# Performance work log

Hardware: AMD Instinct MI355X
Metric: run time of the kernel (lower is better)

## Reference

```python
import jax, jax.numpy as jnp
import numpy as np

D_MODEL = 1024
N_HEADS = 16
D_K = D_MODEL // N_HEADS
SEQ = 2048
BATCH = 2
THETA = 10000.0


def apply_rope(x, positions, theta):
    # x: [..., h, s, d_k], positions: [s]
    d_k = x.shape[-1]
    inv_freq = 1.0 / (theta ** (jnp.arange(0, d_k, 2, dtype=jnp.float32) / d_k))  # [d_k/2]
    ang = positions.astype(jnp.float32)[:, None] * inv_freq[None, :]  # [s, d_k/2]
    cos, sin = jnp.cos(ang), jnp.sin(ang)
    xe, xo = x[..., 0::2], x[..., 1::2]
    re = xe * cos - xo * sin
    ro = xe * sin + xo * cos
    return jnp.stack([re, ro], axis=-1).reshape(x.shape)


def setup_inputs() -> dict:
    key = jax.random.key(0)
    ks = jax.random.split(key, 7)
    f = lambda k, s: jax.random.normal(k, s, dtype=jnp.float32)
    return {
        "Q": f(ks[0], (BATCH, SEQ, D_MODEL)),
        "K": f(ks[1], (BATCH, SEQ, D_MODEL)),
        "V": f(ks[2], (BATCH, SEQ, D_MODEL)),
        "w_q": f(ks[3], (D_MODEL, D_MODEL)) * 0.02,
        "w_k": f(ks[4], (D_MODEL, D_MODEL)) * 0.02,
        "w_v": f(ks[5], (D_MODEL, D_MODEL)) * 0.02,
        "w_o": f(ks[6], (D_MODEL, D_MODEL)) * 0.02,
        "mask": jnp.tril(jnp.ones((SEQ, SEQ), dtype=bool)),
        "token_positions": jnp.arange(SEQ, dtype=jnp.int32),
    }


def reference(Q, K, V, w_q, w_k, w_v, w_o, mask, token_positions):
    h, d_k = N_HEADS, D_K
    # projections: weight is [h*d_k, d_model], applied as x @ W^T
    def proj(x, w):
        y = jnp.einsum('bsd,ed->bse', x, w)
        b, s, _ = y.shape
        return y.reshape(b, s, h, d_k).transpose(0, 2, 1, 3)  # [b,h,s,d_k]
    q = proj(Q, w_q)
    k = proj(K, w_k)
    v = proj(V, w_v)
    q = apply_rope(q, token_positions, THETA)
    k = apply_rope(k, token_positions, THETA)
    scores = jnp.einsum('bhqd,bhkd->bhqk', q, k) / jnp.sqrt(jnp.float32(d_k))
    scores = jnp.where(mask, scores, -jnp.inf)
    attn = jax.nn.softmax(scores, axis=-1)
    out = jnp.einsum('bhqk,bhkd->bhqd', attn, v)
    b, _, s, _ = out.shape
    out = out.transpose(0, 2, 1, 3).reshape(b, s, h * d_k)
    return jnp.einsum('bse,de->bsd', out, w_o)
```

## Files before the change

kernel.cpp:

```cpp
#include <hip/hip_runtime.h>

#define SEQ 2048
#define BATCH 2
#define DM 1024
#define NH 16
#define DK 64
#define BH (BATCH*NH)

typedef __attribute__((ext_vector_type(8))) short bf16x8;
typedef __attribute__((ext_vector_type(4))) float f32x4;

__device__ __forceinline__ ushort f2bf(float f) {
  union { float f; unsigned u; } v; v.f = f;
  unsigned r = (v.u + 0x7fffu + ((v.u >> 16) & 1u)) >> 16;
  return (ushort)r;
}
__device__ __forceinline__ float bf2f(ushort h) {
  union { unsigned u; float f; } v; v.u = ((unsigned)h) << 16;
  return v.f;
}
__device__ __forceinline__ unsigned cvtpk(float lo, float hi) {
  unsigned r;
  asm("v_cvt_pk_bf16_f32 %0, %1, %2" : "=v"(r) : "v"(lo), "v"(hi));
  return r;
}

#define WAITV4 asm volatile("s_waitcnt vmcnt(4)" ::: "memory")
#define WAITV3 asm volatile("s_waitcnt vmcnt(3)" ::: "memory")
#define WAITV0 asm volatile("s_waitcnt vmcnt(0)" ::: "memory")
#define WAITL0 asm volatile("s_waitcnt lgkmcnt(0)" ::: "memory")
#define BARR() __builtin_amdgcn_s_barrier()

struct P4 { const float* p0; const float* p1; const float* p2; const float* p3; };
__global__ void k_castN(P4 in, ushort* __restrict__ out, int n4) {
  const float* src = (blockIdx.z == 0) ? in.p0 : (blockIdx.z == 1) ? in.p1
                    : (blockIdx.z == 2) ? in.p2 : in.p3;
  ushort* dst = out + (size_t)blockIdx.z * (size_t)n4 * 4;
  int i = blockIdx.x * blockDim.x + threadIdx.x;
  int st = gridDim.x * blockDim.x;
  for (; i < n4; i += st) {
    float4 v = reinterpret_cast<const float4*>(src)[i];
    ushort4 o;
    o.x = f2bf(v.x); o.y = f2bf(v.y); o.z = f2bf(v.z); o.w = f2bf(v.w);
    reinterpret_cast<ushort4*>(dst)[i] = o;
  }
}

__global__ void k_rope_tab(float* __restrict__ tab) {
  int id = blockIdx.x * blockDim.x + threadIdx.x;
  if (id >= SEQ * 32) return;
  int s = id >> 5, i = id & 31;
  float inv = powf(10000.f, -(float)i / 32.f);
  float ang = (float)s * inv;
  float sn, cs;
  sincosf(ang, &sn, &cs);
  tab[id * 2] = cs;
  tab[id * 2 + 1] = sn;
}

__global__ __launch_bounds__(256) void k_tr_v(const ushort* __restrict__ Y,
                                              ushort* __restrict__ VT) {
  __shared__ ushort tile[64][65];
  const int st = blockIdx.x, bh = blockIdx.y;
  const int b = bh >> 4, h = bh & 15;
  const int d = threadIdx.x & 63, s4 = threadIdx.x >> 6;
#pragma unroll
  for (int p = 0; p < 16; ++p) {
    int sl = p * 4 + s4;
    tile[d][sl] = Y[(size_t)(b * SEQ + st * 64 + sl) * DM + h * 64 + d];
  }
  __syncthreads();
  const int sl = threadIdx.x & 63, d4 = threadIdx.x >> 6;
#pragma unroll
  for (int p = 0; p < 16; ++p) {
    int dl = p * 4 + d4;
    VT[(size_t)bh * DK * SEQ + (size_t)dl * SEQ + st * 64 + sl] = tile[dl][sl];
  }
}

__device__ __forceinline__ void gll16(const void* g, void* l) {
  __builtin_amdgcn_global_load_lds((const __attribute__((address_space(1))) void*)g,
                                   (__attribute__((address_space(3))) void*)l, 16, 0, 0);
}

#define GSTAGE(AD, BD, kk_) do {                                               \
    gll16(A + (size_t)(m0 + w * 16 + lrow) * K + (kk_) + lcol, (void*)((AD) + w * 512));        \
    gll16(A + (size_t)(m0 + 64 + w * 16 + lrow) * K + (kk_) + lcol, (void*)((AD) + 2048 + w * 512)); \
    gll16(Bw + (size_t)(n0 + w * 16 + lrow) * K + (kk_) + lcol, (void*)((BD) + w * 512));       \
    gll16(Bw + (size_t)(n0 + 64 + w * 16 + lrow) * K + (kk_) + lcol, (void*)((BD) + 2048 + w * 512)); \
  } while (0)

#define GCOMP(AS_, BS_) do {                                                   \
    bf16x8 af[4], bfr[4];                                                      \
    _Pragma("unroll")                                                          \
    for (int i = 0; i < 4; ++i)                                                \
      af[i] = *(const bf16x8*)((AS_) + (wr * 64 + i * 16 + l15) * 32 + l4 * 8);\
    _Pragma("unroll")                                                          \
    for (int i = 0; i < 4; ++i)                                                \
      bfr[i] = *(const bf16x8*)((BS_) + (wc * 64 + i * 16 + l15) * 32 + l4 * 8);\
    _Pragma("unroll")                                                          \
    for (int mi = 0; mi < 4; ++mi)                                             \
      _Pragma("unroll")                                                        \
      for (int ni = 0; ni < 4; ++ni)                                           \
        acc[mi][ni] = __builtin_amdgcn_mfma_f32_16x16x32_bf16(af[mi], bfr[ni], acc[mi][ni], 0, 0, 0); \
  } while (0)

__global__ __launch_bounds__(256) void k_gemm_qkv(const ushort* __restrict__ A,
                                                  const ushort* __restrict__ Bw,
                                                  ushort* __restrict__ qT,
                                                  ushort* __restrict__ kT,
                                                  ushort* __restrict__ YV,
                                                  const float* __restrict__ tab,
                                                  float qscale, int M, int N, int K) {
  const int id = blockIdx.x;
  const int mlo = id & 7, nb = (id >> 3) & 7, mhi = (id >> 6) & 3, z = id >> 8;
  const int m0 = (mhi * 8 + mlo) * 128, n0 = nb * 128;
  A += (size_t)z * ((size_t)M * K);
  Bw += (size_t)z * ((size_t)N * K);
  __shared__ ushort As0[128 * 32], Bs0[128 * 32];
  __shared__ ushort As1[128 * 32], Bs1[128 * 32];
  const int tid = threadIdx.x;
  const int w = tid >> 6, lane = tid & 63;
  const int l15 = lane & 15, l4 = lane >> 4;
  const int wr = w >> 1, wc = w & 1;
  const int lrow = lane >> 2, lcol = (lane & 3) * 8;
  f32x4 acc[4][4] = {};
  GSTAGE(As0, Bs0, 0);
  GSTAGE(As1, Bs1, 32);
  for (int kk = 0; kk < K - 64; kk += 64) {
    WAITV4; BARR();
    GCOMP(As0, Bs0);
    WAITL0; BARR();
    GSTAGE(As0, Bs0, kk + 64);
    WAITV4; BARR();
    GCOMP(As1, Bs1);
    WAITL0; BARR();
    if (kk + 96 < K) GSTAGE(As1, Bs1, kk + 96);
  }
  WAITV4; BARR();
  GCOMP(As0, Bs0);
  WAITV0; BARR();
  GCOMP(As1, Bs1);
  if (z == 2) {
#pragma unroll
    for (int mi = 0; mi < 4; ++mi)
#pragma unroll
      for (int ni = 0; ni < 4; ++ni)
#pragma unroll
        for (int r = 0; r < 4; ++r) {
          int row = m0 + wr * 64 + mi * 16 + l4 * 4 + r;
          int col = n0 + wc * 64 + ni * 16 + l15;
          YV[(size_t)row * N + col] = f2bf(acc[mi][ni][r]);
        }
  } else {
    const float scale = (z == 0) ? qscale : 1.0f;
    ushort* T = (z == 0) ? qT : kT;
    const bool odd = (l15 & 1);
#pragma unroll
    for (int mi = 0; mi < 4; ++mi)
#pragma unroll
      for (int ni = 0; ni < 4; ++ni)
#pragma unroll
        for (int r = 0; r < 4; ++r) {
          int row = m0 + wr * 64 + mi * 16 + l4 * 4 + r;
          int col = n0 + wc * 64 + ni * 16 + l15;
          float v = acc[mi][ni][r];
          float pv = __shfl_xor(v, 1);
          int s = row & (SEQ - 1);
          int d = col & 63;
          float2 cs = *(const float2*)(tab + ((size_t)s * 32 + (d >> 1)) * 2);
          float xe = odd ? pv : v, xo = odd ? v : pv;
          float outv = (odd ? (xe * cs.y + xo * cs.x) : (xe * cs.x - xo * cs.y)) * scale;
          int bh = (row >> 11) * 16 + (col >> 6);
          T[((size_t)bh * SEQ + s) * 64 + d] = f2bf(outv);
        }
  }
}

#define FSTAGE(AD, BD, kk_) do {                                               \
    gll16(A + (size_t)(m0 + srow) * K + (kk_) + scol, (void*)((AD) + w * 512));\
    gll16(Bw + (size_t)(n0 + srow) * K + (kk_) + scol, (void*)((BD) + w * 512));\
    gll16(Bw + (size_t)(n0 + 64 + srow) * K + (kk_) + scol, (void*)((BD) + 2048 + w * 512)); \
  } while (0)

#define FCOMP(AS_, BS_) do {                                                   \
    bf16x8 af[2], bfr[4];                                                      \
    _Pragma("unroll")                                                          \
    for (int i = 0; i < 2; ++i)                                                \
      af[i] = *(const bf16x8*)((AS_) + (wr * 32 + i * 16 + l15) * 32 + l4 * 8);\
    _Pragma("unroll")                                                          \
    for (int i = 0; i < 4; ++i)                                                \
      bfr[i] = *(const bf16x8*)((BS_) + (wc * 64 + i * 16 + l15) * 32 + l4 * 8);\
    _Pragma("unroll")                                                          \
    for (int mi = 0; mi < 2; ++mi)                                             \
      _Pragma("unroll")                                                        \
      for (int ni = 0; ni < 4; ++ni)                                           \
        acc[mi][ni] = __builtin_amdgcn_mfma_f32_16x16x32_bf16(af[mi], bfr[ni], acc[mi][ni], 0, 0, 0); \
  } while (0)

__global__ __launch_bounds__(256) void k_gemm_f(const ushort* __restrict__ A,
                                                const ushort* __restrict__ Bw,
                                                float* __restrict__ C, int M, int N, int K) {
  const int id = blockIdx.x;
  const int mlo = id & 7, nb = (id >> 3) & 7, mhi = id >> 6;
  const int m0 = (mhi * 8 + mlo) * 64, n0 = nb * 128;
  __shared__ ushort As0[64 * 32], Bs0[128 * 32];
  __shared__ ushort As1[64 * 32], Bs1[128 * 32];
  const int tid = threadIdx.x;
  const int w = tid >> 6, lane = tid & 63;
  const int l15 = lane & 15, l4 = lane >> 4;
  const int wr = w >> 1, wc = w & 1;
  const int srow = tid >> 2, scol = (tid & 3) * 8;
  f32x4 acc[2][4] = {};
  FSTAGE(As0, Bs0, 0);
  FSTAGE(As1, Bs1, 32);
  for (int kk = 0; kk < K - 64; kk += 64) {
    WAITV3; BARR();
    FCOMP(As0, Bs0);
    WAITL0; BARR();
    FSTAGE(As0, Bs0, kk + 64);
    WAITV3; BARR();
    FCOMP(As1, Bs1);
    WAITL0; BARR();
    if (kk + 96 < K) FSTAGE(As1, Bs1, kk + 96);
  }
  WAITV3; BARR();
  FCOMP(As0, Bs0);
  WAITV0; BARR();
  FCOMP(As1, Bs1);
#pragma unroll
  for (int mi = 0; mi < 2; ++mi)
#pragma unroll
    for (int ni = 0; ni < 4; ++ni)
#pragma unroll
      for (int r = 0; r < 4; ++r) {
        int row = m0 + wr * 32 + mi * 16 + l4 * 4 + r;
        int col = n0 + wc * 64 + ni * 16 + l15;
        C[(size_t)row * N + col] = acc[mi][ni][r];
      }
}

#define KSTAGE(DST, kt_) do {                                                  \
    const ushort* kb_ = kT + hb + (size_t)(kt_) * 8192;                        \
    _Pragma("unroll")                                                          \
    for (int i_ = 0; i_ < 4; ++i_) {                                           \
      int tt_ = i_ * 256 + tid;                                                \
      int row_ = tt_ >> 3, c_ = (tt_ & 7) ^ (row_ & 7);                        \
      gll16(kb_ + (size_t)row_ * 64 + c_ * 8,                                  \
            (void*)((char*)(DST) + (i_ * 256 + w * 64) * 16));                 \
    }                                                                          \
  } while (0)

#define VSTAGE(DST, kt_) do {                                                  \
    const ushort* vb_ = vT + vbase + (size_t)(kt_) * 128;                      \
    _Pragma("unroll")                                                          \
    for (int i_ = 0; i_ < 4; ++i_) {                                           \
      int tt_ = i_ * 256 + tid;                                                \
      int row_ = tt_ >> 4, c_ = (tt_ & 15) ^ (row_ & 15);                      \
      gll16(vb_ + (size_t)row_ * SEQ + c_ * 8,                                 \
            (void*)((char*)(DST) + (i_ * 256 + w * 64) * 16));                 \
    }                                                                          \
  } while (0)

#define FRK(BASE, row_, cidx)                                                  \
  (*(const bf16x8*)((const char*)(BASE) + (row_) * 128 + ((((cidx) ^ ((row_) & 7)) & 7) * 16)))
#define FRV(BASE, row_, cidx)                                                  \
  (*(const bf16x8*)((const char*)(BASE) + (row_) * 256 + ((((cidx) ^ ((row_) & 15)) & 15) * 16)))

#define SMAX8(P, MRUN, LRUN, ACC) do {                                         \
    float mx = P[0][0];                                                        \
    _Pragma("unroll")                                                          \
    for (int nf = 0; nf < 8; ++nf)                                             \
      _Pragma("unroll")                                                        \
      for (int r = 0; r < 4; ++r) mx = fmaxf(mx, P[nf][r]);                    \
    mx = fmaxf(mx, __shfl_xor(mx, 16));                                        \
    mx = fmaxf(mx, __shfl_xor(mx, 32));                                        \
    if (!__all(mx <= MRUN)) {                                                  \
      const float mn = fmaxf(MRUN, mx);                                        \
      const float so = __builtin_amdgcn_exp2f(MRUN - mn);                      \
      float soq[4];                                                            \
      _Pragma("unroll")                                                        \
      for (int r = 0; r < 4; ++r) soq[r] = __shfl(so, l4 * 4 + r);             \
      _Pragma("unroll")                                                        \
      for (int df = 0; df < 4; ++df)                                           \
        _Pragma("unroll")                                                      \
        for (int r = 0; r < 4; ++r) ACC[df][r] *= soq[r];                      \
      LRUN *= so;                                                              \
      MRUN = mn;                                                               \
    }                                                                          \
    float rs = 0.f;                                                            \
    _Pragma("unroll")                                                          \
    for (int nf = 0; nf < 8; ++nf) {                                           \
      float e0 = __builtin_amdgcn_exp2f(P[nf][0] - MRUN);                      \
      float e1 = __builtin_amdgcn_exp2f(P[nf][1] - MRUN);                      \
      float e2 = __builtin_amdgcn_exp2f(P[nf][2] - MRUN);                      \
      float e3 = __builtin_amdgcn_exp2f(P[nf][3] - MRUN);                      \
      P[nf][0] = e0; P[nf][1] = e1; P[nf][2] = e2; P[nf][3] = e3;              \
      rs += (e0 + e1) + (e2 + e3);                                             \
    }                                                                          \
    LRUN += rs;                                                                \
  } while (0)

#define PVHALF(P, MYP, ACC, VC, H) do {                                        \
    _Pragma("unroll")                                                          \
    for (int i = 0; i < 4; ++i) {                                              \
      uint2 pk;                                                                \
      pk.x = cvtpk(P[(H) * 4 + i][0], P[(H) * 4 + i][1]);                      \
      pk.y = cvtpk(P[(H) * 4 + i][2], P[(H) * 4 + i][3]);                      \
      *(uint2*)((MYP) + ((l15 * 128 + i * 32 + l4 * 8) ^ swz)) = pk;           \
    }                                                                          \
    const bf16x8 pa0 = *(const bf16x8*)((MYP) + ((l15 * 128 + l4 * 16) ^ swz));\
    const bf16x8 pa1 = *(const bf16x8*)((MYP) + ((l15 * 128 + 64 + l4 * 16) ^ swz));\
    _Pragma("unroll")                                                          \
    for (int df = 0; df < 4; ++df) {                                           \
      bf16x8 v0_ = FRV(VC, df * 16 + l15, (H) * 8 + l4);                       \
      bf16x8 v1_ = FRV(VC, df * 16 + l15, (H) * 8 + l4 + 4);                   \
      ACC[df] = __builtin_amdgcn_mfma_f32_16x16x32_bf16(pa0, v0_, ACC[df], 0, 0, 0); \
      ACC[df] = __builtin_amdgcn_mfma_f32_16x16x32_bf16(pa1, v1_, ACC[df], 0, 0, 0); \
    }                                                                          \
  } while (0)

#define STEP(KC, VC, KN, VN, kt_, DIAG, PREF) do {                             \
    if (PREF) { KSTAGE(KN, (kt_) + 1); VSTAGE(VN, (kt_) + 1); }                \
    float p0[8][4], p1[8][4];                                                  \
    _Pragma("unroll")                                                          \
    for (int nf = 0; nf < 8; ++nf) {                                           \
      bf16x8 k0_ = FRK(KC, nf * 16 + l15, l4);                                 \
      bf16x8 k1_ = FRK(KC, nf * 16 + l15, l4 + 4);                             \
      if (!(DIAG) || nf < 4) {                                                 \
        f32x4 z = {0.f, 0.f, 0.f, 0.f};                                        \
        z = __builtin_amdgcn_mfma_f32_16x16x32_bf16(k0_, qb00, z, 0, 0, 0);    \
        z = __builtin_amdgcn_mfma_f32_16x16x32_bf16(k1_, qb01, z, 0, 0, 0);    \
        _Pragma("unroll")                                                      \
        for (int r = 0; r < 4; ++r) {                                          \
          float sc = z[r];                                                     \
          if (DIAG && (nf * 16 + l4 * 4 + r) > (w * 16 + l15)) sc = -INFINITY; \
          p0[nf][r] = sc;                                                      \
        }                                                                      \
      } else {                                                                 \
        _Pragma("unroll")                                                      \
        for (int r = 0; r < 4; ++r) p0[nf][r] = -INFINITY;                     \
      }                                                                        \
      {                                                                        \
        f32x4 z = {0.f, 0.f, 0.f, 0.f};                                        \
        z = __builtin_amdgcn_mfma_f32_16x16x32_bf16(k0_, qb10, z, 0, 0, 0);    \
        z = __builtin_amdgcn_mfma_f32_16x16x32_bf16(k1_, qb11, z, 0, 0, 0);    \
        _Pragma("unroll")                                                      \
        for (int r = 0; r < 4; ++r) {                                          \
          float sc = z[r];                                                     \
          if (DIAG && (nf * 16 + l4 * 4 + r) > (64 + w * 16 + l15)) sc = -INFINITY; \
          p1[nf][r] = sc;                                                      \
        }                                                                      \
      }                                                                        \
    }                                                                          \
    SMAX8(p0, mrun0, lrun0, acc0);                                             \
    SMAX8(p1, mrun1, lrun1, acc1);                                             \
    PVHALF(p0, myP0, acc0, VC, 0);                                             \
    if (!(DIAG)) PVHALF(p0, myP0, acc0, VC, 1);                                \
    PVHALF(p1, myP1, acc1, VC, 0);                                             \
    PVHALF(p1, myP1, acc1, VC, 1);                                             \
    __syncthreads();                                                           \
  } while (0)

__global__ __launch_bounds__(256, 2) void k_flash(const ushort* __restrict__ qT,
                                                  const ushort* __restrict__ kT,
                                                  const ushort* __restrict__ vT,
                                                  ushort* __restrict__ AO) {
  __shared__ ushort Ks[2][128 * 64];
  __shared__ ushort Vs[2][64 * 128];
  __shared__ char Plds[4 * 4096];
  const int l = blockIdx.x;
  const int bh = (l & 7) * 4 + ((l >> 3) & 3);
  const int qt = (SEQ / 128 - 1) - (l >> 5);
  const int tid = threadIdx.x, w = tid >> 6, lane = tid & 63;
  const int l15 = lane & 15, l4 = lane >> 4;
  const size_t hb = (size_t)bh * SEQ * DK;
  const size_t vbase = (size_t)bh * DK * SEQ;
  const int qrow0 = qt * 128 + w * 16;
  const int qrow1 = qrow0 + 64;
  const bf16x8 qb00 = *(const bf16x8*)(qT + hb + (size_t)(qrow0 + l15) * 64 + l4 * 8);
  const bf16x8 qb01 = *(const bf16x8*)(qT + hb + (size_t)(qrow0 + l15) * 64 + 32 + l4 * 8);
  const bf16x8 qb10 = *(const bf16x8*)(qT + hb + (size_t)(qrow1 + l15) * 64 + l4 * 8);
  const bf16x8 qb11 = *(const bf16x8*)(qT + hb + (size_t)(qrow1 + l15) * 64 + 32 + l4 * 8);
  f32x4 acc0[4] = {}, acc1[4] = {};
  float mrun0 = -INFINITY, lrun0 = 0.f, mrun1 = -INFINITY, lrun1 = 0.f;
  char* myP0 = (char*)Plds + w * 4096;
  char* myP1 = myP0 + 2048;
  const int swz = (l15 & 7) << 4;
  ushort* kc = &Ks[0][0]; ushort* vc = &Vs[0][0];
  ushort* kn = &Ks[1][0]; ushort* vn = &Vs[1][0];
  KSTAGE(kc, 0); VSTAGE(vc, 0);
  __syncthreads();
  for (int kt = 0; kt < qt; ++kt) {
    STEP(kc, vc, kn, vn, kt, false, true);
    ushort* t;
    t = kc; kc = kn; kn = t;
    t = vc; vc = vn; vn = t;
  }
  STEP(kc, vc, kn, vn, qt, true, false);
  lrun0 += __shfl_xor(lrun0, 16); lrun0 += __shfl_xor(lrun0, 32);
  lrun1 += __shfl_xor(lrun1, 16); lrun1 += __shfl_xor(lrun1, 32);
  const int b = bh >> 4, h = bh & 15;
  float lq0[4], lq1[4];
#pragma unroll
  for (int r = 0; r < 4; ++r) {
    lq0[r] = __shfl(lrun0, l4 * 4 + r);
    lq1[r] = __shfl(lrun1, l4 * 4 + r);
  }
#pragma unroll
  for (int r = 0; r < 4; ++r) {
    float inv0 = 1.f / lq0[r], inv1 = 1.f / lq1[r];
    int qr0 = qrow0 + l4 * 4 + r, qr1 = qrow1 + l4 * 4 + r;
#pragma unroll
    for (int df = 0; df < 4; ++df) {
      AO[(size_t)(b * SEQ + qr0) * DM + h * 64 + df * 16 + l15] = f2bf(acc0[df][r] * inv0);
      AO[(size_t)(b * SEQ + qr1) * DM + h * 64 + df * 16 + l15] = f2bf(acc1[df][r] * inv1);
    }
  }
}

extern "C" void kernel_launch(void* const* d_in, const int* in_sizes, int n_in,
                              void* d_out, int out_size, void* d_ws, size_t ws_size,
                              hipStream_t stream) {
  const float* Q = (const float*)d_in[0];
  const float* K = (const float*)d_in[1];
  const float* V = (const float*)d_in[2];
  const float* wq = (const float*)d_in[3];
  const float* wk = (const float*)d_in[4];
  const float* wv = (const float*)d_in[5];
  const float* wo = (const float*)d_in[6];
  float* out = (float*)d_out;
  char* ws = (char*)d_ws;

  ushort* XQ = (ushort*)(ws + 0);
  ushort* XK = (ushort*)(ws + 8388608);
  ushort* WQ = (ushort*)(ws + 25165824);
  ushort* qT = (ushort*)(ws + 33554432);
  ushort* kT = (ushort*)(ws + 41943040);
  ushort* YV = (ushort*)(ws + 50331648);
  float* TAB = (float*)(ws + 58720256);
  ushort* vT = XQ;
  ushort* AO = XK;

  const int NX4 = BATCH * SEQ * DM / 4;
  const int NW4 = DM * DM / 4;
  P4 xin = {Q, K, V, nullptr};
  P4 win = {wq, wk, wv, wo};
  k_castN<<<dim3(1024, 1, 3), 256, 0, stream>>>(xin, XQ, NX4);
  k_castN<<<dim3(1024, 1, 4), 256, 0, stream>>>(win, WQ, NW4);
  k_rope_tab<<<(SEQ * 32) / 256, 256, 0, stream>>>(TAB);

  const float QSCALE = 0.125f * 1.4426950408889634f;
  k_gemm_qkv<<<768, 256, 0, stream>>>(XQ, WQ, qT, kT, YV, TAB, QSCALE,
                                      BATCH * SEQ, DM, DM);

  k_tr_v<<<dim3(SEQ / 64, BH), 256, 0, stream>>>(YV, vT);

  k_flash<<<BH * (SEQ / 128), 256, 0, stream>>>(qT, kT, vT, AO);

  k_gemm_f<<<512, 256, 0, stream>>>(AO, WQ + 3 * DM * DM, out, BATCH * SEQ, DM, DM);
}
```

Baseline: 127.0 us.

## Fuse activation fp32-to-bf16 cast and V transpose into QKV GEMM

The QKV projection GEMM now reads the fp32 Q/K/V activations directly, converts them to bf16 in registers and writes them into LDS, with a register-prefetch pipeline replacing the async global-to-LDS loads for A. The V output is written straight into the transposed [bh, d, s] layout, so the separate activation cast kernel and the V transpose kernel go away, along with their launches and global round trips. In exchange the GEMM reads twice the A bytes in fp32, uses more registers for prefetch, and the V stores become strided scatters.

```diff
diff --git a/kernel.cpp b/kernel.cpp
--- a/kernel.cpp
+++ b/kernel.cpp
@@ -27,6 +27,7 @@
 
 #define WAITV4 asm volatile("s_waitcnt vmcnt(4)" ::: "memory")
 #define WAITV3 asm volatile("s_waitcnt vmcnt(3)" ::: "memory")
+#define WAITV2 asm volatile("s_waitcnt vmcnt(2)" ::: "memory")
 #define WAITV0 asm volatile("s_waitcnt vmcnt(0)" ::: "memory")
 #define WAITL0 asm volatile("s_waitcnt lgkmcnt(0)" ::: "memory")
 #define BARR() __builtin_amdgcn_s_barrier()
@@ -58,34 +59,34 @@
   tab[id * 2 + 1] = sn;
 }
 
-__global__ __launch_bounds__(256) void k_tr_v(const ushort* __restrict__ Y,
-                                              ushort* __restrict__ VT) {
-  __shared__ ushort tile[64][65];
-  const int st = blockIdx.x, bh = blockIdx.y;
-  const int b = bh >> 4, h = bh & 15;
-  const int d = threadIdx.x & 63, s4 = threadIdx.x >> 6;
-#pragma unroll
-  for (int p = 0; p < 16; ++p) {
-    int sl = p * 4 + s4;
-    tile[d][sl] = Y[(size_t)(b * SEQ + st * 64 + sl) * DM + h * 64 + d];
-  }
-  __syncthreads();
-  const int sl = threadIdx.x & 63, d4 = threadIdx.x >> 6;
-#pragma unroll
-  for (int p = 0; p < 16; ++p) {
-    int dl = p * 4 + d4;
-    VT[(size_t)bh * DK * SEQ + (size_t)dl * SEQ + st * 64 + sl] = tile[dl][sl];
-  }
-}
-
 __device__ __forceinline__ void gll16(const void* g, void* l) {
   __builtin_amdgcn_global_load_lds((const __attribute__((address_space(1))) void*)g,
                                    (__attribute__((address_space(3))) void*)l, 16, 0, 0);
 }
 
-#define GSTAGE(AD, BD, kk_) do {                                               \
-    gll16(A + (size_t)(m0 + w * 16 + lrow) * K + (kk_) + lcol, (void*)((AD) + w * 512));        \
-    gll16(A + (size_t)(m0 + 64 + w * 16 + lrow) * K + (kk_) + lcol, (void*)((AD) + 2048 + w * 512)); \
+#define LOADA(R, kk_) do {                                                     \
+    _Pragma("unroll")                                                          \
+    for (int i_ = 0; i_ < 2; ++i_) {                                           \
+      int row_ = i_ * 64 + (tid >> 2), c_ = (tid & 3) * 8;                     \
+      const float4* s_ = (const float4*)(Afp + (size_t)(m0 + row_) * K + (kk_) + c_); \
+      R[2 * i_] = s_[0]; R[2 * i_ + 1] = s_[1];                                \
+    }                                                                          \
+  } while (0)
+
+#define AWRITE(AD, R) do {                                                     \
+    _Pragma("unroll")                                                          \
+    for (int i_ = 0; i_ < 2; ++i_) {                                           \
+      int row_ = i_ * 64 + (tid >> 2), c_ = (tid & 3) * 8;                     \
+      uint4 pk_;                                                               \
+      pk_.x = cvtpk(R[2 * i_].x, R[2 * i_].y);                                 \
+      pk_.y = cvtpk(R[2 * i_].z, R[2 * i_].w);                                 \
+      pk_.z = cvtpk(R[2 * i_ + 1].x, R[2 * i_ + 1].y);                         \
+      pk_.w = cvtpk(R[2 * i_ + 1].z, R[2 * i_ + 1].w);                         \
+      *(uint4*)((AD) + row_ * 32 + c_) = pk_;                                  \
+    }                                                                          \
+  } while (0)
+
+#define GLLB(BD, kk_) do {                                                     \
     gll16(Bw + (size_t)(n0 + w * 16 + lrow) * K + (kk_) + lcol, (void*)((BD) + w * 512));       \
     gll16(Bw + (size_t)(n0 + 64 + w * 16 + lrow) * K + (kk_) + lcol, (void*)((BD) + 2048 + w * 512)); \
   } while (0)
@@ -105,18 +106,30 @@
         acc[mi][ni] = __builtin_amdgcn_mfma_f32_16x16x32_bf16(af[mi], bfr[ni], acc[mi][ni], 0, 0, 0); \
   } while (0)
 
-__global__ __launch_bounds__(256) void k_gemm_qkv(const ushort* __restrict__ A,
-                                                  const ushort* __restrict__ Bw,
+#define PHASE(CAS, CBS, NAS, NBS, RIN, ROUT, T2OK, t_) do {                    \
+    GLLB(NBS, ((t_) + 1) * 32);                                                \
+    WAITV2;                                                                    \
+    AWRITE(NAS, RIN);                                                          \
+    if (T2OK) LOADA(ROUT, ((t_) + 2) * 32);                                    \
+    GCOMP(CAS, CBS);                                                           \
+    if (T2OK) { WAITV4; } else { WAITV0; }                                     \
+    WAITL0; BARR();                                                            \
+  } while (0)
+
+__global__ __launch_bounds__(256) void k_gemm_qkv(const float* __restrict__ Qf,
+                                                  const float* __restrict__ Kf,
+                                                  const float* __restrict__ Vf,
+                                                  const ushort* __restrict__ Bw0,
                                                   ushort* __restrict__ qT,
                                                   ushort* __restrict__ kT,
-                                                  ushort* __restrict__ YV,
+                                                  ushort* __restrict__ vT,
                                                   const float* __restrict__ tab,
                                                   float qscale, int M, int N, int K) {
   const int id = blockIdx.x;
   const int mlo = id & 7, nb = (id >> 3) & 7, mhi = (id >> 6) & 3, z = id >> 8;
   const int m0 = (mhi * 8 + mlo) * 128, n0 = nb * 128;
-  A += (size_t)z * ((size_t)M * K);
-  Bw += (size_t)z * ((size_t)N * K);
+  const float* Afp = (z == 0) ? Qf : (z == 1) ? Kf : Vf;
+  const ushort* Bw = Bw0 + (size_t)z * ((size_t)N * K);
   __shared__ ushort As0[128 * 32], Bs0[128 * 32];
   __shared__ ushort As1[128 * 32], Bs1[128 * 32];
   const int tid = threadIdx.x;
@@ -124,22 +137,19 @@
   const int l15 = lane & 15, l4 = lane >> 4;
   const int wr = w >> 1, wc = w & 1;
   const int lrow = lane >> 2, lcol = (lane & 3) * 8;
+  float4 rA[4], rB[4];
   f32x4 acc[4][4] = {};
-  GSTAGE(As0, Bs0, 0);
-  GSTAGE(As1, Bs1, 32);
-  for (int kk = 0; kk < K - 64; kk += 64) {
-    WAITV4; BARR();
-    GCOMP(As0, Bs0);
-    WAITL0; BARR();
-    GSTAGE(As0, Bs0, kk + 64);
-    WAITV4; BARR();
-    GCOMP(As1, Bs1);
-    WAITL0; BARR();
-    if (kk + 96 < K) GSTAGE(As1, Bs1, kk + 96);
-  }
-  WAITV4; BARR();
-  GCOMP(As0, Bs0);
-  WAITV0; BARR();
+  LOADA(rA, 0);
+  GLLB(Bs0, 0);
+  WAITV0;
+  AWRITE(As0, rA);
+  LOADA(rB, 32);
+  WAITL0; BARR();
+  for (int t = 0; t < 30; t += 2) {
+    PHASE(As0, Bs0, As1, Bs1, rB, rA, 1, t);
+    PHASE(As1, Bs1, As0, Bs0, rA, rB, 1, t + 1);
+  }
+  PHASE(As0, Bs0, As1, Bs1, rB, rA, 0, 30);
   GCOMP(As1, Bs1);
   if (z == 2) {
 #pragma unroll
@@ -150,7 +160,9 @@
         for (int r = 0; r < 4; ++r) {
           int row = m0 + wr * 64 + mi * 16 + l4 * 4 + r;
           int col = n0 + wc * 64 + ni * 16 + l15;
-          YV[(size_t)row * N + col] = f2bf(acc[mi][ni][r]);
+          int bh2 = (row >> 11) * 16 + (col >> 6);
+          int d = col & 63, s = row & (SEQ - 1);
+          vT[((size_t)bh2 * 64 + d) * SEQ + s] = f2bf(acc[mi][ni][r]);
         }
   } else {
     const float scale = (z == 0) ? qscale : 1.0f;
@@ -171,8 +183,8 @@
           float2 cs = *(const float2*)(tab + ((size_t)s * 32 + (d >> 1)) * 2);
           float xe = odd ? pv : v, xo = odd ? v : pv;
           float outv = (odd ? (xe * cs.y + xo * cs.x) : (xe * cs.x - xo * cs.y)) * scale;
-          int bh = (row >> 11) * 16 + (col >> 6);
-          T[((size_t)bh * SEQ + s) * 64 + d] = f2bf(outv);
+          int bh2 = (row >> 11) * 16 + (col >> 6);
+          T[((size_t)bh2 * SEQ + s) * 64 + d] = f2bf(outv);
         }
   }
 }
@@ -432,30 +444,22 @@
   float* out = (float*)d_out;
   char* ws = (char*)d_ws;
 
-  ushort* XQ = (ushort*)(ws + 0);
-  ushort* XK = (ushort*)(ws + 8388608);
+  ushort* qT = (ushort*)(ws + 0);
+  ushort* kT = (ushort*)(ws + 8388608);
+  ushort* vT = (ushort*)(ws + 16777216);
   ushort* WQ = (ushort*)(ws + 25165824);
-  ushort* qT = (ushort*)(ws + 33554432);
-  ushort* kT = (ushort*)(ws + 41943040);
-  ushort* YV = (ushort*)(ws + 50331648);
-  float* TAB = (float*)(ws + 58720256);
-  ushort* vT = XQ;
-  ushort* AO = XK;
-
-  const int NX4 = BATCH * SEQ * DM / 4;
+  ushort* AO = (ushort*)(ws + 33554432);
+  float* TAB = (float*)(ws + 41943040);
+
   const int NW4 = DM * DM / 4;
-  P4 xin = {Q, K, V, nullptr};
   P4 win = {wq, wk, wv, wo};
-  k_castN<<<dim3(1024, 1, 3), 256, 0, stream>>>(xin, XQ, NX4);
   k_castN<<<dim3(1024, 1, 4), 256, 0, stream>>>(win, WQ, NW4);
   k_rope_tab<<<(SEQ * 32) / 256, 256, 0, stream>>>(TAB);
 
   const float QSCALE = 0.125f * 1.4426950408889634f;
-  k_gemm_qkv<<<768, 256, 0, stream>>>(XQ, WQ, qT, kT, YV, TAB, QSCALE,
+  k_gemm_qkv<<<768, 256, 0, stream>>>(Q, K, V, WQ, qT, kT, vT, TAB, QSCALE,
                                       BATCH * SEQ, DM, DM);
 
-  k_tr_v<<<dim3(SEQ / 64, BH), 256, 0, stream>>>(YV, vT);
-
   k_flash<<<BH * (SEQ / 128), 256, 0, stream>>>(qT, kT, vT, AO);
 
   k_gemm_f<<<512, 256, 0, stream>>>(AO, WQ + 3 * DM * DM, out, BATCH * SEQ, DM, DM);
```

New measurement: 120.0 us. -5.5%, faster.
